# Optimization experiments

Measured on AMD Instinct MI355X. Metric: run time of the kernel, lower is better.

Reference implementation:

```python
import jax, jax.numpy as jnp
import numpy as np


def setup_inputs() -> dict:
    key = jax.random.key(0)
    features = jax.random.normal(key, (32, 512, 64, 64), dtype=jnp.float32)
    return {"features": features}


def reference(features):
    # Faithful SPPNet forward: for k in {1,2,3}, partition the spatial map into
    # k x k blocks of size (h//k, w//k) (trailing remainder ignored), and take
    # the max over the ENTIRE slice (batch, channel, and spatial dims),
    # yielding one scalar per block: 1 + 4 + 9 = 14 values, shape [1, 14].
    b, c, h, w = features.shape
    outs = []
    for k in (1, 2, 3):
        gh, gw = h // k, w // k
        # [b, c, k, gh, k, gw]; block (i, j) = x[:, :, i, :, j, :]
        x = features[:, :, : gh * k, : gw * k].reshape(b, c, k, gh, k, gw)
        m = jnp.max(x, axis=(0, 1, 3, 5))  # [k, k], row-major (i, j) order
        outs.append(m.reshape(-1))
    return jnp.concatenate(outs)[None, :]  # [1, 14]
```

## Files before the change

kernel.cpp:

```cpp
#include <hip/hip_runtime.h>
#include <math.h>


#define IMG_F4 1024
#define IMGS_PER_BLOCK 16
#define MAIN_BLOCKS 1024
#define NBIN 14

__device__ __forceinline__ void fmax4(float4& m, const float4 v) {
    m.x = fmaxf(m.x, v.x);
    m.y = fmaxf(m.y, v.y);
    m.z = fmaxf(m.z, v.z);
    m.w = fmaxf(m.w, v.w);
}

__global__ __launch_bounds__(1024, 8)
void spp_main(const float4* __restrict__ in, float* __restrict__ P2) {
    const int t = threadIdx.x;
    const long long base = (long long)blockIdx.x * (IMGS_PER_BLOCK * IMG_F4) + t;

    float4 m0 = in[base + 0 * IMG_F4];
    float4 m1 = in[base + 1 * IMG_F4];
    float4 m2 = in[base + 2 * IMG_F4];
    float4 m3 = in[base + 3 * IMG_F4];
    #pragma unroll
    for (int img = 4; img < IMGS_PER_BLOCK; img += 4) {
        fmax4(m0, in[base + (long long)(img + 0) * IMG_F4]);
        fmax4(m1, in[base + (long long)(img + 1) * IMG_F4]);
        fmax4(m2, in[base + (long long)(img + 2) * IMG_F4]);
        fmax4(m3, in[base + (long long)(img + 3) * IMG_F4]);
    }
    fmax4(m0, m1);
    fmax4(m2, m3);
    fmax4(m0, m2);

    __shared__ float sm[4096];
    *(float4*)&sm[t * 4] = m0;
    __syncthreads();

    const int q = t >> 6;
    const int l = t & 63;
    if (q < NBIN) {
        float best = -INFINITY;
        if (q == 0) {
            float b0 = -INFINITY, b1 = -INFINITY, b2 = -INFINITY, b3 = -INFINITY;
            #pragma unroll
            for (int i = 0; i < 64; i += 4) {
                b0 = fmaxf(b0, sm[(i + 0) * 64 + l]);
                b1 = fmaxf(b1, sm[(i + 1) * 64 + l]);
                b2 = fmaxf(b2, sm[(i + 2) * 64 + l]);
                b3 = fmaxf(b3, sm[(i + 3) * 64 + l]);
            }
            best = fmaxf(fmaxf(b0, b1), fmaxf(b2, b3));
        } else if (q < 5) {
            const int b = q - 1;
            const int rs = (b >> 1) * 32;
            float b0 = -INFINITY, b1 = -INFINITY, b2 = -INFINITY, b3 = -INFINITY;
            #pragma unroll
            for (int i = 0; i < 32; i += 4) {
                b0 = fmaxf(b0, sm[(rs + i + 0) * 64 + l]);
                b1 = fmaxf(b1, sm[(rs + i + 1) * 64 + l]);
                b2 = fmaxf(b2, sm[(rs + i + 2) * 64 + l]);
                b3 = fmaxf(b3, sm[(rs + i + 3) * 64 + l]);
            }
            best = fmaxf(fmaxf(b0, b1), fmaxf(b2, b3));
            if ((l >> 5) != (b & 1)) best = -INFINITY;
        } else {
            const int b = q - 5;
            const int rs = (b / 3) * 21;
            float b0 = -INFINITY, b1 = -INFINITY, b2 = -INFINITY;
            #pragma unroll
            for (int i = 0; i < 21; i += 3) {
                b0 = fmaxf(b0, sm[(rs + i + 0) * 64 + l]);
                b1 = fmaxf(b1, sm[(rs + i + 1) * 64 + l]);
                b2 = fmaxf(b2, sm[(rs + i + 2) * 64 + l]);
            }
            best = fmaxf(b0, fmaxf(b1, b2));
            if (!(l < 63 && (l / 21) == (b % 3))) best = -INFINITY;
        }

        #pragma unroll
        for (int off = 32; off > 0; off >>= 1)
            best = fmaxf(best, __shfl_down(best, off, 64));

        if (l == 0) P2[q * MAIN_BLOCKS + blockIdx.x] = best;
    }
}

__global__ __launch_bounds__(1024)
void spp_final(const float* __restrict__ P2, float* __restrict__ out) {
    const int q = threadIdx.x >> 6;
    const int l = threadIdx.x & 63;
    if (q >= NBIN) return;

    float best = -INFINITY;
    #pragma unroll
    for (int j = 0; j < MAIN_BLOCKS; j += 64)
        best = fmaxf(best, P2[q * MAIN_BLOCKS + j + l]);

    #pragma unroll
    for (int off = 32; off > 0; off >>= 1)
        best = fmaxf(best, __shfl_down(best, off, 64));

    if (l == 0) out[q] = best;
}

extern "C" void kernel_launch(void* const* d_in, const int* in_sizes, int n_in,
                              void* d_out, int out_size, void* d_ws, size_t ws_size,
                              hipStream_t stream) {
    const float4* in = (const float4*)d_in[0];
    float* out = (float*)d_out;
    float* P2 = (float*)d_ws;

    spp_main<<<MAIN_BLOCKS, 1024, 0, stream>>>(in, P2);
    spp_final<<<1, 1024, 0, stream>>>(P2, out);
}
```

Measured before the change: 49.53 us.

## Fuse final reduction into main kernel via hierarchical last-block atomic counters

Replaces the separate final-reduction kernel with a last-block-done pattern: each block stores its partial maxima, increments one of eight sharded counters, and the block that completes the last group performs the final 14-bin reduction. Counters are zeroed with a memset before launch. This removes a second kernel launch and its dependency gap, but adds a memset node, atomics, and an extra __syncthreads per block.

```diff
diff --git a/kernel.cpp b/kernel.cpp
--- a/kernel.cpp
+++ b/kernel.cpp
@@ -6,6 +6,14 @@
 #define IMGS_PER_BLOCK 16
 #define MAIN_BLOCKS 1024
 #define NBIN 14
+#define NGRP 8
+#define GRP_SIZE (MAIN_BLOCKS / NGRP)
+
+#define P2_FLOATS (NBIN * MAIN_BLOCKS)
+#define CTR_BASE_BYTES (P2_FLOATS * 4)
+#define CTR_STRIDE_INT 64
+#define CTR2_IDX (NGRP * CTR_STRIDE_INT)
+#define MEMSET_BYTES ((NGRP * CTR_STRIDE_INT + 1) * 4 + 60)
 
 __device__ __forceinline__ void fmax4(float4& m, const float4 v) {
     m.x = fmaxf(m.x, v.x);
@@ -15,7 +23,8 @@
 }
 
 __global__ __launch_bounds__(1024, 8)
-void spp_main(const float4* __restrict__ in, float* __restrict__ P2) {
+void spp_fused(const float4* __restrict__ in, float* __restrict__ P2,
+               int* __restrict__ ctrs, float* __restrict__ out) {
     const int t = threadIdx.x;
     const long long base = (long long)blockIdx.x * (IMGS_PER_BLOCK * IMG_F4) + t;
 
@@ -35,6 +44,7 @@
     fmax4(m0, m2);
 
     __shared__ float sm[4096];
+    __shared__ int sLast;
     *(float4*)&sm[t * 4] = m0;
     __syncthreads();
 
@@ -83,26 +93,37 @@
         for (int off = 32; off > 0; off >>= 1)
             best = fmaxf(best, __shfl_down(best, off, 64));
 
-        if (l == 0) P2[q * MAIN_BLOCKS + blockIdx.x] = best;
+        if (l == 0)
+            __hip_atomic_store(&P2[q * MAIN_BLOCKS + blockIdx.x], best,
+                               __ATOMIC_RELAXED, __HIP_MEMORY_SCOPE_AGENT);
     }
-}
 
-__global__ __launch_bounds__(1024)
-void spp_final(const float* __restrict__ P2, float* __restrict__ out) {
-    const int q = threadIdx.x >> 6;
-    const int l = threadIdx.x & 63;
-    if (q >= NBIN) return;
+    __syncthreads();
+    if (t == 0) {
+        int last = 0;
+        const int g = blockIdx.x & (NGRP - 1);
+        int o1 = __hip_atomic_fetch_add(&ctrs[g * CTR_STRIDE_INT], 1,
+                                        __ATOMIC_ACQ_REL, __HIP_MEMORY_SCOPE_AGENT);
+        if (o1 == GRP_SIZE - 1) {
+            int o2 = __hip_atomic_fetch_add(&ctrs[CTR2_IDX], 1,
+                                            __ATOMIC_ACQ_REL, __HIP_MEMORY_SCOPE_AGENT);
+            last = (o2 == NGRP - 1);
+        }
+        sLast = last;
+    }
+    __syncthreads();
 
-    float best = -INFINITY;
-    #pragma unroll
-    for (int j = 0; j < MAIN_BLOCKS; j += 64)
-        best = fmaxf(best, P2[q * MAIN_BLOCKS + j + l]);
-
-    #pragma unroll
-    for (int off = 32; off > 0; off >>= 1)
-        best = fmaxf(best, __shfl_down(best, off, 64));
-
-    if (l == 0) out[q] = best;
+    if (sLast && q < NBIN) {
+        float best = -INFINITY;
+        #pragma unroll
+        for (int j = 0; j < MAIN_BLOCKS; j += 64)
+            best = fmaxf(best, __hip_atomic_load(&P2[q * MAIN_BLOCKS + j + l],
+                         __ATOMIC_RELAXED, __HIP_MEMORY_SCOPE_AGENT));
+        #pragma unroll
+        for (int off = 32; off > 0; off >>= 1)
+            best = fmaxf(best, __shfl_down(best, off, 64));
+        if (l == 0) out[q] = best;
+    }
 }
 
 extern "C" void kernel_launch(void* const* d_in, const int* in_sizes, int n_in,
@@ -111,7 +132,8 @@
     const float4* in = (const float4*)d_in[0];
     float* out = (float*)d_out;
     float* P2 = (float*)d_ws;
+    int* ctrs = (int*)((char*)d_ws + CTR_BASE_BYTES);
 
-    spp_main<<<MAIN_BLOCKS, 1024, 0, stream>>>(in, P2);
-    spp_final<<<1, 1024, 0, stream>>>(P2, out);
+    hipMemsetAsync((char*)d_ws + CTR_BASE_BYTES, 0, MEMSET_BYTES, stream);
+    spp_fused<<<MAIN_BLOCKS, 1024, 0, stream>>>(in, P2, ctrs, out);
 }
```

New measurement: 78.71 us. 1.59x slower.
